# Optimization experiments

Hardware: AMD Instinct MI355X
Metric: run time of the kernel (lower is better)

Reference implementation:

```python
import jax, jax.numpy as jnp
import numpy as np

EMBED_DIM = 1024
NUM_HEADS = 16
HEAD_DIM = EMBED_DIM // NUM_HEADS
SCALE = HEAD_DIM ** -0.5


def setup_inputs() -> dict:
    key = jax.random.key(0)
    ks = jax.random.split(key, 9)
    B, N, C = 4, 2048, EMBED_DIM
    w_std = C ** -0.5
    return {
        "x": jax.random.normal(ks[0], (B, N, C), dtype=jnp.float32),
        "w_q": jax.random.normal(ks[1], (C, C), dtype=jnp.float32) * w_std,
        "b_q": jax.random.normal(ks[2], (C,), dtype=jnp.float32) * 0.02,
        "w_k": jax.random.normal(ks[3], (C, C), dtype=jnp.float32) * w_std,
        "b_k": jax.random.normal(ks[4], (C,), dtype=jnp.float32) * 0.02,
        "w_v": jax.random.normal(ks[5], (C, C), dtype=jnp.float32) * w_std,
        "b_v": jax.random.normal(ks[6], (C,), dtype=jnp.float32) * 0.02,
        "w_o": jax.random.normal(ks[7], (C, C), dtype=jnp.float32) * w_std,
        "b_o": jax.random.normal(ks[8], (C,), dtype=jnp.float32) * 0.02,
    }


def reference(x, w_q, b_q, w_k, b_k, w_v, b_v, w_o, b_o):
    B, N, C = x.shape
    H, D = NUM_HEADS, HEAD_DIM
    # qkv projections (nn.Linear: x @ W^T + b); weights stored as (out, in) -> use W directly as (in,out) by generating square random; math identical
    q = (x @ w_q + b_q).reshape(B, N, H, D).transpose(0, 2, 1, 3)  # bhnd
    k = (x @ w_k + b_k).reshape(B, N, H, D).transpose(0, 2, 1, 3)
    v = (x @ w_v + b_v).reshape(B, N, H, D).transpose(0, 2, 1, 3)
    attn = jnp.einsum("bhnd,bhmd->bhnm", q, k) * SCALE
    attn = jax.nn.softmax(attn, axis=-1)  # dropout p=0.0 -> identity
    out = jnp.einsum("bhnm,bhmd->bhnd", attn, v)
    out = out.transpose(0, 2, 1, 3).reshape(B, N, C)
    return out @ w_o + b_o
```

## Files before the change

kernel.cpp:

```cpp
#include <hip/hip_runtime.h>
#include <math.h>

constexpr float SOFTMAX_OFF = 6.0f;
constexpr float LOG2E = 1.44269504088896f;

using half4  = __attribute__((ext_vector_type(4))) _Float16;
using half8  = __attribute__((ext_vector_type(8))) _Float16;
using floatx4 = __attribute__((ext_vector_type(4))) float;

__device__ __forceinline__ void gll16(const _Float16* src, _Float16* dst) {
  __builtin_amdgcn_global_load_lds((const __attribute__((address_space(1))) void*)src,
                                   (__attribute__((address_space(3))) void*)dst, 16, 0, 0);
}
__device__ __forceinline__ float exp2_fast(float x) {
#if __has_builtin(__builtin_amdgcn_exp2f)
  return __builtin_amdgcn_exp2f(x);
#else
  float r; asm("v_exp_f32 %0, %1" : "=v"(r) : "v"(x)); return r;
#endif
}

__device__ __forceinline__ int gsw(int row) { return ((row >> 3) ^ row) & 7; }
__device__ __forceinline__ int gsw8(int row, int chunk) {
  return row * 64 + ((chunk ^ gsw(row)) << 3);
}

__device__ __forceinline__ void stage_tile(const _Float16* __restrict__ src,
                                           _Float16* lds, int tid) {
  const int w = tid >> 6, l = tid & 63;
#pragma unroll
  for (int i = 0; i < 4; i++) {
    const int rbase = w * 8 + i * 32;
    const int row = rbase + (l >> 3);
    const int chunk = (l & 7) ^ gsw(row);
    gll16(src + (size_t)row * 1024 + chunk * 8, lds + rbase * 64);
  }
}

__device__ __forceinline__ void mfma_core16(const _Float16* __restrict__ A,
                                            const _Float16* __restrict__ B,
                                            _Float16* As, _Float16* Bs,
                                            floatx4 (&acc)[4][4]) {
  const int tid = threadIdx.x;
  const int lane = tid & 63;
  const int w = tid >> 6;
  const int wrow = w >> 1, wcol = w & 1;
  const int quad = lane >> 4, lm = lane & 15;

  for (int k0 = 0; k0 < 1024; k0 += 64) {
    stage_tile(A + k0, As, tid);
    stage_tile(B + k0, Bs, tid);
    __syncthreads();

    half8 af[4][2], bf[4][2];
#pragma unroll
    for (int mi = 0; mi < 4; mi++) {
      int row = wrow * 64 + mi * 16 + lm;
      af[mi][0] = *(const half8*)&As[gsw8(row, quad)];
      af[mi][1] = *(const half8*)&As[gsw8(row, 4 + quad)];
    }
#pragma unroll
    for (int nj = 0; nj < 4; nj++) {
      int row = wcol * 64 + nj * 16 + lm;
      bf[nj][0] = *(const half8*)&Bs[gsw8(row, quad)];
      bf[nj][1] = *(const half8*)&Bs[gsw8(row, 4 + quad)];
    }
    __builtin_amdgcn_s_setprio(1);
#pragma unroll
    for (int mi = 0; mi < 4; mi++)
#pragma unroll
      for (int nj = 0; nj < 4; nj++) {
        acc[mi][nj] = __builtin_amdgcn_mfma_f32_16x16x32_f16(af[mi][0], bf[nj][0], acc[mi][nj], 0, 0, 0);
        acc[mi][nj] = __builtin_amdgcn_mfma_f32_16x16x32_f16(af[mi][1], bf[nj][1], acc[mi][nj], 0, 0, 0);
      }
    __builtin_amdgcn_s_setprio(0);
    __syncthreads();
  }
}

__global__ __launch_bounds__(256) void gemm_qkv_mfma(
    const _Float16* __restrict__ xh, const _Float16* __restrict__ WT,
    const float* __restrict__ bq, const float* __restrict__ bk, const float* __restrict__ bv,
    _Float16* __restrict__ Oq, _Float16* __restrict__ Ok, _Float16* __restrict__ Ov) {
  __shared__ __align__(16) _Float16 SM[128 * 128];
  _Float16* As = SM;
  _Float16* Bs = SM + 128 * 64;

  const int sel = blockIdx.x >> 3;
  const int colBase = (blockIdx.x & 7) * 128;
  const int rowBase = blockIdx.y * 128;
  const float* bias = (sel == 0) ? bq : (sel == 1) ? bk : bv;
  const _Float16* Bp = WT + (size_t)sel * 1048576 + (size_t)colBase * 1024;

  floatx4 acc[4][4];
#pragma unroll
  for (int mi = 0; mi < 4; mi++)
#pragma unroll
    for (int nj = 0; nj < 4; nj++) acc[mi][nj] = (floatx4){0.f, 0.f, 0.f, 0.f};

  mfma_core16(xh + (size_t)rowBase * 1024, Bp, As, Bs, acc);

  const int tid = threadIdx.x;
  const int lane = tid & 63;
  const int w = tid >> 6;
  const int wrow = w >> 1, wcol = w & 1;
  const int quad = lane >> 4, lm = lane & 15;

  if (sel < 2) {
    _Float16* out = (sel == 0) ? Oq : Ok;
#pragma unroll
    for (int nj = 0; nj < 4; nj++) {
      int col = colBase + wcol * 64 + nj * 16 + lm;
      float bv_ = bias[col];
      int h = col >> 6, d = col & 63;
#pragma unroll
      for (int mi = 0; mi < 4; mi++) {
        int row0 = rowBase + wrow * 64 + mi * 16 + quad * 4;
#pragma unroll
        for (int r = 0; r < 4; r++) {
          int row = row0 + r;
          int bb = row >> 11, n = row & 2047;
          out[((size_t)((bb * 16 + h) * 2048 + n)) * 64 + d] = (_Float16)(acc[mi][nj][r] + bv_);
        }
      }
    }
  } else {
#pragma unroll
    for (int nj = 0; nj < 4; nj++) {
      int colp = wcol * 64 + nj * 16 + lm;
      float bv_ = bias[colBase + colp];
#pragma unroll
      for (int mi = 0; mi < 4; mi++) {
        int row0 = wrow * 64 + mi * 16 + quad * 4;
#pragma unroll
        for (int r = 0; r < 4; r++) {
          int rowp = row0 + r;
          SM[colp * 128 + ((((rowp >> 3) ^ (colp & 15))) << 3) + (rowp & 7)] =
              (_Float16)(acc[mi][nj][r] + bv_);
        }
      }
    }
    __syncthreads();
    const int b = rowBase >> 11, n0 = rowBase & 2047;
    const int ci = tid & 15;
#pragma unroll
    for (int i = 0; i < 8; i++) {
      int c = (tid >> 4) * 8 + i;
      half8 hv = *(const half8*)&SM[c * 128 + ((ci ^ (c & 15)) << 3)];
      int col = colBase + c;
      int hh = col >> 6, d = col & 63;
      *(half8*)&Ov[((size_t)(b * 16 + hh) * 64 + d) * 2048 + n0 + ci * 8] = hv;
    }
  }
}

__global__ __launch_bounds__(256) void gemm_out_mfma(const _Float16* __restrict__ A,
                                                     const _Float16* __restrict__ WT,
                                                     const float* __restrict__ bias,
                                                     float* __restrict__ out) {
  __shared__ __align__(16) _Float16 SM[128 * 128];
  _Float16* As = SM;
  _Float16* Bs = SM + 128 * 64;

  const int colBase = blockIdx.x * 128;
  const int rowBase = blockIdx.y * 128;

  floatx4 acc[4][4];
#pragma unroll
  for (int mi = 0; mi < 4; mi++)
#pragma unroll
    for (int nj = 0; nj < 4; nj++) acc[mi][nj] = (floatx4){0.f, 0.f, 0.f, 0.f};

  mfma_core16(A + (size_t)rowBase * 1024, WT + (size_t)colBase * 1024, As, Bs, acc);

  const int tid = threadIdx.x;
  const int lane = tid & 63;
  const int w = tid >> 6;
  const int wrow = w >> 1, wcol = w & 1;
  const int quad = lane >> 4, lm = lane & 15;

#pragma unroll
  for (int nj = 0; nj < 4; nj++) {
    int col = colBase + wcol * 64 + nj * 16 + lm;
    float bv_ = bias[col];
#pragma unroll
    for (int mi = 0; mi < 4; mi++) {
      int row0 = rowBase + wrow * 64 + mi * 16 + quad * 4;
#pragma unroll
      for (int r = 0; r < 4; r++)
        out[(size_t)(row0 + r) * 1024 + col] = acc[mi][nj][r] + bv_;
    }
  }
}

__global__ __launch_bounds__(256) void prepass(const float* __restrict__ x,
                                               const float* __restrict__ w_q,
                                               const float* __restrict__ w_k,
                                               const float* __restrict__ w_v,
                                               _Float16* __restrict__ xh,
                                               _Float16* __restrict__ WTqkv) {
  const int bx = blockIdx.x;
  const int tid = threadIdx.x;
  if (bx < 768) {
    __shared__ float tile[64][65];
    const int wsel = bx >> 8, t = bx & 255;
    const float* W = (wsel == 0) ? w_q : (wsel == 1) ? w_k : w_v;
    _Float16* out = WTqkv + (size_t)wsel * 1048576;
    const int n0 = (t & 15) * 64, k0 = (t >> 4) * 64;
#pragma unroll
    for (int i = 0; i < 16; i++) {
      int idx = tid + i * 256;
      int r = idx >> 6, c = idx & 63;
      tile[r][c] = W[(size_t)(k0 + r) * 1024 + n0 + c];
    }
    __syncthreads();
#pragma unroll
    for (int i = 0; i < 4; i++) {
      int r = (tid >> 4) + i * 16;
      int c0 = (tid & 15) * 4;
      half4 h = {(_Float16)tile[c0][r], (_Float16)tile[c0 + 1][r],
                 (_Float16)tile[c0 + 2][r], (_Float16)tile[c0 + 3][r]};
      *(half4*)&out[(size_t)(n0 + r) * 1024 + k0 + c0] = h;
    }
  } else {
    int idx = ((bx - 768) * 256 + tid) * 8;
    float4 a = *(const float4*)(x + idx);
    float4 b = *(const float4*)(x + idx + 4);
    half8 h = {(_Float16)a.x, (_Float16)a.y, (_Float16)a.z, (_Float16)a.w,
               (_Float16)b.x, (_Float16)b.y, (_Float16)b.z, (_Float16)b.w};
    *(half8*)(xh + idx) = h;
  }
}

__global__ __launch_bounds__(256) void transpose_wo(const float* __restrict__ W,
                                                    _Float16* __restrict__ out) {
  __shared__ float tile[64][65];
  const int n0 = blockIdx.x * 64, k0 = blockIdx.y * 64;
  const int tid = threadIdx.x;
#pragma unroll
  for (int i = 0; i < 16; i++) {
    int idx = tid + i * 256;
    int r = idx >> 6, c = idx & 63;
    tile[r][c] = W[(size_t)(k0 + r) * 1024 + n0 + c];
  }
  __syncthreads();
#pragma unroll
  for (int i = 0; i < 4; i++) {
    int r = (tid >> 4) + i * 16;
    int c0 = (tid & 15) * 4;
    half4 h = {(_Float16)tile[c0][r], (_Float16)tile[c0 + 1][r],
               (_Float16)tile[c0 + 2][r], (_Float16)tile[c0 + 3][r]};
    *(half4*)&out[(size_t)(n0 + r) * 1024 + k0 + c0] = h;
  }
}

__device__ __forceinline__ int sw8(int row, int chunk) {
  return row * 64 + ((chunk ^ (row & 7)) << 3);
}

__global__ __launch_bounds__(256, 3) void flash_attn_mfma(const _Float16* __restrict__ Q,
                                                          const _Float16* __restrict__ K,
                                                          const _Float16* __restrict__ VT,
                                                          _Float16* __restrict__ out) {
  __shared__ __align__(16) _Float16 QPs[128 * 64];
  __shared__ __align__(16) _Float16 Ks[2 * 64 * 64];
  __shared__ __align__(16) _Float16 Vs[2 * 64 * 64];

  const int tid = threadIdx.x;
  const int lane = tid & 63;
  const int w = tid >> 6;
  const int quad = lane >> 4, lm = lane & 15;
  const int bh = blockIdx.y;
  const int qbase = blockIdx.x * 128;
  const int b = bh >> 4, h = bh & 15;

  const _Float16* Qp = Q + ((size_t)bh * 2048 + qbase) * 64;
  const _Float16* Kp = K + (size_t)bh * 2048 * 64;
  const _Float16* VTp = VT + (size_t)bh * 2048 * 64;

  const int soff = ((lane & 7) ^ (lane >> 3)) * 8;
  const int srow = w * 8 + (lane >> 3);

#pragma unroll
  for (int i = 0; i < 4; i++)
    gll16(Qp + (size_t)(srow + 32 * i) * 64 + soff, QPs + (w * 8 + 32 * i) * 64);
  const _Float16* kptr = Kp + srow * 64 + soff;
  const _Float16* vptr = VTp + srow * 2048 + soff;
  gll16(kptr, Ks + (w * 8) * 64);
  gll16(kptr + 32 * 64, Ks + (w * 8 + 32) * 64);
  gll16(vptr, Vs + (w * 8) * 64);
  gll16(vptr + 32 * 2048, Vs + (w * 8 + 32) * 64);
  kptr += 64 * 64;
  vptr += 64;
  __syncthreads();

  half8 aq[2][2];
#pragma unroll
  for (int s = 0; s < 2; s++) {
    aq[s][0] = *(const half8*)&QPs[sw8(32 * w + 16 * s + lm, quad)];
    aq[s][1] = *(const half8*)&QPs[sw8(32 * w + 16 * s + lm, 4 + quad)];
  }
  _Float16* Ps = QPs;

  int pb[2][4];
#pragma unroll
  for (int s = 0; s < 2; s++)
#pragma unroll
    for (int r = 0; r < 4; r++) {
      int row = 32 * w + 16 * s + quad * 4 + r;
      pb[s][r] = row * 64 + (lm & 7) + (((lm >> 3) ^ (row & 1)) << 3) +
                 (((row >> 1) & 3) << 4);
    }

  floatx4 o_acc[2][4];
  floatx4 l_acc[2];
#pragma unroll
  for (int s = 0; s < 2; s++) {
    l_acc[s] = (floatx4){0.f, 0.f, 0.f, 0.f};
#pragma unroll
    for (int dt = 0; dt < 4; dt++) o_acc[s][dt] = (floatx4){0.f, 0.f, 0.f, 0.f};
  }
  const half8 vone = {(_Float16)1.f, (_Float16)1.f, (_Float16)1.f, (_Float16)1.f,
                      (_Float16)1.f, (_Float16)1.f, (_Float16)1.f, (_Float16)1.f};

  constexpr float SCL = 0.125f * LOG2E;
  constexpr float OFFC = -SOFTMAX_OFF * LOG2E;

  int cur = 0;
  for (int kt = 0; kt < 32; kt++) {
    if (kt + 1 < 32) {
      _Float16* kd = Ks + (cur ^ 1) * 4096;
      _Float16* vd = Vs + (cur ^ 1) * 4096;
      gll16(kptr, kd + (w * 8) * 64);
      gll16(kptr + 32 * 64, kd + (w * 8 + 32) * 64);
      gll16(vptr, vd + (w * 8) * 64);
      gll16(vptr + 32 * 2048, vd + (w * 8 + 32) * 64);
      kptr += 64 * 64;
      vptr += 64;
    }
    const _Float16* ksC = Ks + cur * 4096;
    const _Float16* vsC = Vs + cur * 4096;

    floatx4 s_acc[2][4];
    __builtin_amdgcn_s_setprio(1);
#pragma unroll
    for (int t = 0; t < 4; t++) {
      half8 bk0 = *(const half8*)&ksC[sw8(16 * t + lm, quad)];
      half8 bk1 = *(const half8*)&ksC[sw8(16 * t + lm, 4 + quad)];
#pragma unroll
      for (int s = 0; s < 2; s++) {
        floatx4 acc = (floatx4){0.f, 0.f, 0.f, 0.f};
        acc = __builtin_amdgcn_mfma_f32_16x16x32_f16(aq[s][0], bk0, acc, 0, 0, 0);
        acc = __builtin_amdgcn_mfma_f32_16x16x32_f16(aq[s][1], bk1, acc, 0, 0, 0);
        s_acc[s][t] = acc;
      }
    }
    __builtin_amdgcn_s_setprio(0);

#pragma unroll
    for (int s = 0; s < 2; s++)
#pragma unroll
      for (int t = 0; t < 4; t++)
#pragma unroll
        for (int r = 0; r < 4; r++)
          Ps[pb[s][r] ^ (t << 4)] = (_Float16)exp2_fast(fmaf(s_acc[s][t][r], SCL, OFFC));

    half8 ap[2][2];
#pragma unroll
    for (int s = 0; s < 2; s++) {
      ap[s][0] = *(const half8*)&Ps[sw8(32 * w + 16 * s + lm, quad)];
      ap[s][1] = *(const half8*)&Ps[sw8(32 * w + 16 * s + lm, 4 + quad)];
    }
    __builtin_amdgcn_s_setprio(1);
#pragma unroll
    for (int dt = 0; dt < 4; dt++) {
      half8 bv0 = *(const half8*)&vsC[sw8(16 * dt + lm, quad)];
      half8 bv1 = *(const half8*)&vsC[sw8(16 * dt + lm, 4 + quad)];
#pragma unroll
      for (int s = 0; s < 2; s++) {
        o_acc[s][dt] = __builtin_amdgcn_mfma_f32_16x16x32_f16(ap[s][0], bv0, o_acc[s][dt], 0, 0, 0);
        o_acc[s][dt] = __builtin_amdgcn_mfma_f32_16x16x32_f16(ap[s][1], bv1, o_acc[s][dt], 0, 0, 0);
      }
    }
#pragma unroll
    for (int s = 0; s < 2; s++) {
      l_acc[s] = __builtin_amdgcn_mfma_f32_16x16x32_f16(ap[s][0], vone, l_acc[s], 0, 0, 0);
      l_acc[s] = __builtin_amdgcn_mfma_f32_16x16x32_f16(ap[s][1], vone, l_acc[s], 0, 0, 0);
    }
    __builtin_amdgcn_s_setprio(0);

    cur ^= 1;
    __syncthreads();
  }

#pragma unroll
  for (int s = 0; s < 2; s++)
#pragma unroll
    for (int r = 0; r < 4; r++) {
      float inv = 1.f / l_acc[s][r];
      int n = qbase + 32 * w + 16 * s + quad * 4 + r;
      _Float16* op = out + ((size_t)(b * 2048 + n)) * 1024 + h * 64;
#pragma unroll
      for (int dt = 0; dt < 4; dt++) op[lm + 16 * dt] = (_Float16)(o_acc[s][dt][r] * inv);
    }
}

extern "C" void kernel_launch(void* const* d_in, const int* in_sizes, int n_in,
                              void* d_out, int out_size, void* d_ws, size_t ws_size,
                              hipStream_t stream) {
  const float* x   = (const float*)d_in[0];
  const float* w_q = (const float*)d_in[1];
  const float* b_q = (const float*)d_in[2];
  const float* w_k = (const float*)d_in[3];
  const float* b_k = (const float*)d_in[4];
  const float* w_v = (const float*)d_in[5];
  const float* b_v = (const float*)d_in[6];
  const float* w_o = (const float*)d_in[7];
  const float* b_o = (const float*)d_in[8];
  float* out = (float*)d_out;

  _Float16* wsh = (_Float16*)d_ws;
  _Float16* Ab = wsh;
  _Float16* Qb = wsh + 8388608;
  _Float16* Kb = wsh + 2 * 8388608;
  _Float16* Vb = wsh + 3 * 8388608;
  _Float16* xh = Ab;
  _Float16* WTqkv = (_Float16*)d_out;
  _Float16* WoT = Qb;

  dim3 blk(256);
  prepass<<<dim3(4864), blk, 0, stream>>>(x, w_q, w_k, w_v, xh, WTqkv);
  gemm_qkv_mfma<<<dim3(24, 64), blk, 0, stream>>>(xh, WTqkv, b_q, b_k, b_v, Qb, Kb, Vb);
  flash_attn_mfma<<<dim3(16, 64), blk, 0, stream>>>(Qb, Kb, Vb, Ab);
  transpose_wo<<<dim3(16, 16), blk, 0, stream>>>(w_o, WoT);
  gemm_out_mfma<<<dim3(8, 64), blk, 0, stream>>>(Ab, WoT, b_o, out);
}
```

Baseline: 296.8 us.

## Keep softmax probabilities in registers via transposed S MFMA, drop LDS round-trip

The QK^T MFMA operands are swapped so each lane holds a transposed score tile. The fp16-packed probabilities can then feed the PV product directly as 16x16x16 MFMA operands, with no store to and reload from LDS. V fragments are read with precomputed swizzled half4 offsets, the row-sum uses the same register operands, and the output is written as half4 vectors. This removes LDS write/read traffic and bank pressure for P. In exchange it uses twice as many smaller MFMAs and changes rounding to round-toward-zero packing.

```diff
diff --git a/kernel.cpp b/kernel.cpp
--- a/kernel.cpp
+++ b/kernel.cpp
@@ -4,6 +4,7 @@
 constexpr float SOFTMAX_OFF = 6.0f;
 constexpr float LOG2E = 1.44269504088896f;
 
+using half2v = __attribute__((ext_vector_type(2))) _Float16;
 using half4  = __attribute__((ext_vector_type(4))) _Float16;
 using half8  = __attribute__((ext_vector_type(8))) _Float16;
 using floatx4 = __attribute__((ext_vector_type(4))) float;
@@ -300,17 +301,6 @@
     aq[s][0] = *(const half8*)&QPs[sw8(32 * w + 16 * s + lm, quad)];
     aq[s][1] = *(const half8*)&QPs[sw8(32 * w + 16 * s + lm, 4 + quad)];
   }
-  _Float16* Ps = QPs;
-
-  int pb[2][4];
-#pragma unroll
-  for (int s = 0; s < 2; s++)
-#pragma unroll
-    for (int r = 0; r < 4; r++) {
-      int row = 32 * w + 16 * s + quad * 4 + r;
-      pb[s][r] = row * 64 + (lm & 7) + (((lm >> 3) ^ (row & 1)) << 3) +
-                 (((row >> 1) & 3) << 4);
-    }
 
   floatx4 o_acc[2][4];
   floatx4 l_acc[2];
@@ -320,11 +310,19 @@
 #pragma unroll
     for (int dt = 0; dt < 4; dt++) o_acc[s][dt] = (floatx4){0.f, 0.f, 0.f, 0.f};
   }
-  const half8 vone = {(_Float16)1.f, (_Float16)1.f, (_Float16)1.f, (_Float16)1.f,
-                      (_Float16)1.f, (_Float16)1.f, (_Float16)1.f, (_Float16)1.f};
+  const half4 vone = {(_Float16)1.f, (_Float16)1.f, (_Float16)1.f, (_Float16)1.f};
 
   constexpr float SCL = 0.125f * LOG2E;
   constexpr float OFFC = -SOFTMAX_OFF * LOG2E;
+
+  int voff[4][4];
+#pragma unroll
+  for (int dt = 0; dt < 4; dt++)
+#pragma unroll
+    for (int t = 0; t < 4; t++) {
+      int row = 16 * dt + lm;
+      voff[dt][t] = row * 64 + (((2 * t + (quad >> 1)) ^ (row & 7)) << 3) + (quad & 1) * 4;
+    }
 
   int cur = 0;
   for (int kt = 0; kt < 32; kt++) {
@@ -341,7 +339,7 @@
     const _Float16* ksC = Ks + cur * 4096;
     const _Float16* vsC = Vs + cur * 4096;
 
-    floatx4 s_acc[2][4];
+    floatx4 st[2][4];
     __builtin_amdgcn_s_setprio(1);
 #pragma unroll
     for (int t = 0; t < 4; t++) {
@@ -350,43 +348,44 @@
 #pragma unroll
       for (int s = 0; s < 2; s++) {
         floatx4 acc = (floatx4){0.f, 0.f, 0.f, 0.f};
-        acc = __builtin_amdgcn_mfma_f32_16x16x32_f16(aq[s][0], bk0, acc, 0, 0, 0);
-        acc = __builtin_amdgcn_mfma_f32_16x16x32_f16(aq[s][1], bk1, acc, 0, 0, 0);
-        s_acc[s][t] = acc;
+        acc = __builtin_amdgcn_mfma_f32_16x16x32_f16(bk0, aq[s][0], acc, 0, 0, 0);
+        acc = __builtin_amdgcn_mfma_f32_16x16x32_f16(bk1, aq[s][1], acc, 0, 0, 0);
+        st[s][t] = acc;
       }
     }
     __builtin_amdgcn_s_setprio(0);
 
+    half4 pf[2][4];
 #pragma unroll
     for (int s = 0; s < 2; s++)
 #pragma unroll
+      for (int t = 0; t < 4; t++) {
+        float p0 = exp2_fast(fmaf(st[s][t][0], SCL, OFFC));
+        float p1 = exp2_fast(fmaf(st[s][t][1], SCL, OFFC));
+        float p2 = exp2_fast(fmaf(st[s][t][2], SCL, OFFC));
+        float p3 = exp2_fast(fmaf(st[s][t][3], SCL, OFFC));
+        half2v lo = __builtin_bit_cast(half2v, __builtin_amdgcn_cvt_pkrtz(p0, p1));
+        half2v hi = __builtin_bit_cast(half2v, __builtin_amdgcn_cvt_pkrtz(p2, p3));
+        pf[s][t] = (half4){lo[0], lo[1], hi[0], hi[1]};
+      }
+
+    __builtin_amdgcn_s_setprio(1);
+#pragma unroll
+    for (int dt = 0; dt < 4; dt++) {
+      half4 vf[4];
+#pragma unroll
+      for (int t = 0; t < 4; t++) vf[t] = *(const half4*)&vsC[voff[dt][t]];
+#pragma unroll
       for (int t = 0; t < 4; t++)
 #pragma unroll
-        for (int r = 0; r < 4; r++)
-          Ps[pb[s][r] ^ (t << 4)] = (_Float16)exp2_fast(fmaf(s_acc[s][t][r], SCL, OFFC));
-
-    half8 ap[2][2];
-#pragma unroll
-    for (int s = 0; s < 2; s++) {
-      ap[s][0] = *(const half8*)&Ps[sw8(32 * w + 16 * s + lm, quad)];
-      ap[s][1] = *(const half8*)&Ps[sw8(32 * w + 16 * s + lm, 4 + quad)];
-    }
-    __builtin_amdgcn_s_setprio(1);
-#pragma unroll
-    for (int dt = 0; dt < 4; dt++) {
-      half8 bv0 = *(const half8*)&vsC[sw8(16 * dt + lm, quad)];
-      half8 bv1 = *(const half8*)&vsC[sw8(16 * dt + lm, 4 + quad)];
-#pragma unroll
-      for (int s = 0; s < 2; s++) {
-        o_acc[s][dt] = __builtin_amdgcn_mfma_f32_16x16x32_f16(ap[s][0], bv0, o_acc[s][dt], 0, 0, 0);
-        o_acc[s][dt] = __builtin_amdgcn_mfma_f32_16x16x32_f16(ap[s][1], bv1, o_acc[s][dt], 0, 0, 0);
-      }
-    }
-#pragma unroll
-    for (int s = 0; s < 2; s++) {
-      l_acc[s] = __builtin_amdgcn_mfma_f32_16x16x32_f16(ap[s][0], vone, l_acc[s], 0, 0, 0);
-      l_acc[s] = __builtin_amdgcn_mfma_f32_16x16x32_f16(ap[s][1], vone, l_acc[s], 0, 0, 0);
-    }
+        for (int s = 0; s < 2; s++)
+          o_acc[s][dt] = __builtin_amdgcn_mfma_f32_16x16x16f16(vf[t], pf[s][t], o_acc[s][dt], 0, 0, 0);
+    }
+#pragma unroll
+    for (int s = 0; s < 2; s++)
+#pragma unroll
+      for (int t = 0; t < 4; t++)
+        l_acc[s] = __builtin_amdgcn_mfma_f32_16x16x16f16(vone, pf[s][t], l_acc[s], 0, 0, 0);
     __builtin_amdgcn_s_setprio(0);
 
     cur ^= 1;
@@ -394,15 +393,17 @@
   }
 
 #pragma unroll
-  for (int s = 0; s < 2; s++)
-#pragma unroll
-    for (int r = 0; r < 4; r++) {
-      float inv = 1.f / l_acc[s][r];
-      int n = qbase + 32 * w + 16 * s + quad * 4 + r;
-      _Float16* op = out + ((size_t)(b * 2048 + n)) * 1024 + h * 64;
-#pragma unroll
-      for (int dt = 0; dt < 4; dt++) op[lm + 16 * dt] = (_Float16)(o_acc[s][dt][r] * inv);
-    }
+  for (int s = 0; s < 2; s++) {
+    float inv = 1.f / l_acc[s][0];
+    int n = qbase + 32 * w + 16 * s + lm;
+    _Float16* op = out + ((size_t)(b * 2048 + n)) * 1024 + h * 64 + quad * 4;
+#pragma unroll
+    for (int dt = 0; dt < 4; dt++) {
+      half4 hv = {(_Float16)(o_acc[s][dt][0] * inv), (_Float16)(o_acc[s][dt][1] * inv),
+                  (_Float16)(o_acc[s][dt][2] * inv), (_Float16)(o_acc[s][dt][3] * inv)};
+      *(half4*)&op[16 * dt] = hv;
+    }
+  }
 }
 
 extern "C" void kernel_launch(void* const* d_in, const int* in_sizes, int n_in,
```

New measurement: 298.8 us. About the same (+0.7%).
